# Kernel optimization log

Hardware: AMD Instinct MI355X
Metric: run time of the kernel (lower is better)

Reference implementation:

```python
import jax, jax.numpy as jnp
import numpy as np

N = 50000
R = 8
E = 100000
D_IN = 768
D_H = 256
LN_EPS = 1e-5


def _layer_norm(h, g, b):
    mu = jnp.mean(h, axis=-1, keepdims=True)
    var = jnp.mean((h - mu) ** 2, axis=-1, keepdims=True)
    return (h - mu) * jax.lax.rsqrt(var + LN_EPS) * g + b


def _rgcn_layer(x, node_w, edge_src, edge_tgt, W_rel, W_self_w, W_self_b, ln_g, ln_b):
    # x: [N, d_in]; edge_src/edge_tgt: [R, E]; W_rel: [R, d_in, d_out]
    n = x.shape[0]
    out = x @ W_self_w + W_self_b  # self loop
    for r in range(W_rel.shape[0]):  # fixed, small relation count
        src = edge_src[r]
        tgt = edge_tgt[r]
        feats = x[src] * node_w[src][:, None]          # gather + nuclearity scale, [E, d_in]
        msg = feats @ W_rel[r]                          # per-relation linear, [E, d_out]
        agg = jax.ops.segment_sum(msg, tgt, num_segments=n)                 # scatter_add
        cnt = jax.ops.segment_sum(jnp.ones(src.shape[0], x.dtype), tgt, num_segments=n)
        out = out + agg / jnp.clip(cnt, 1.0)[:, None]  # mean over relation neighbors
    return _layer_norm(jax.nn.relu(out), ln_g, ln_b)   # dropout = identity (eval)


def setup_inputs() -> dict:
    key = jax.random.key(0)
    ks = jax.random.split(key, 10)
    x = jax.random.normal(ks[0], (N, D_IN), dtype=jnp.float32)
    node_weights = jax.random.uniform(ks[1], (N,), dtype=jnp.float32)
    edge_src = jax.random.randint(ks[2], (R, E), 0, N, dtype=jnp.int32)
    edge_tgt = jax.random.randint(ks[3], (R, E), 0, N, dtype=jnp.int32)
    W_rel0 = jax.random.normal(ks[4], (R, D_IN, D_H), dtype=jnp.float32) / np.sqrt(D_IN)
    W_self0_w = jax.random.normal(ks[5], (D_IN, D_H), dtype=jnp.float32) / np.sqrt(D_IN)
    W_self0_b = jnp.zeros((D_H,), jnp.float32)
    W_rel1 = jax.random.normal(ks[6], (R, D_H, D_H), dtype=jnp.float32) / np.sqrt(D_H)
    W_self1_w = jax.random.normal(ks[7], (D_H, D_H), dtype=jnp.float32) / np.sqrt(D_H)
    W_self1_b = jnp.zeros((D_H,), jnp.float32)
    ones = jnp.ones((D_H,), jnp.float32)
    zeros = jnp.zeros((D_H,), jnp.float32)
    return {
        "x": x, "node_weights": node_weights,
        "edge_src": edge_src, "edge_tgt": edge_tgt,
        "W_rel0": W_rel0, "W_self0_w": W_self0_w, "W_self0_b": W_self0_b,
        "ln0_g": ones, "ln0_b": zeros,
        "W_rel1": W_rel1, "W_self1_w": W_self1_w, "W_self1_b": W_self1_b,
        "ln1_g": ones, "ln1_b": zeros,
    }


def reference(x, node_weights, edge_src, edge_tgt,
              W_rel0, W_self0_w, W_self0_b, ln0_g, ln0_b,
              W_rel1, W_self1_w, W_self1_b, ln1_g, ln1_b):
    h = _rgcn_layer(x, node_weights, edge_src, edge_tgt,
                    W_rel0, W_self0_w, W_self0_b, ln0_g, ln0_b)
    h = _rgcn_layer(h, node_weights, edge_src, edge_tgt,
                    W_rel1, W_self1_w, W_self1_b, ln1_g, ln1_b)
    return h  # [N, 256]
```

## Files before the change

### kernel.cpp

```cpp
#include <hip/hip_runtime.h>
#include <stdint.h>

#define N_NODES 50000
#define M_PAD   50048
#define R_REL   8
#define E_EDGES 100000
#define D_IN    768
#define D_H     256
#define N_CAT   2304
#define LN_EPS  1e-5f

#define TILES_N 18
#define TILES_M 391
#define T_TOT   (TILES_N * TILES_M)
#define T_PER_XCD ((T_TOT + 7) / 8)
#define NCHUNK  49
#define EP_STRIDE 68
#define E_PAD_MAX 960000

typedef __attribute__((ext_vector_type(8))) __bf16        bf16x8;
typedef __attribute__((ext_vector_type(4))) float         f32x4;
typedef __attribute__((ext_vector_type(8))) unsigned short u16x8;
typedef __attribute__((ext_vector_type(4))) unsigned short u16x4;
typedef __attribute__((ext_vector_type(4))) int            i32x4;

__device__ __forceinline__ float bf2f(unsigned short u) {
  union { float f; uint32_t i; } c; c.i = ((uint32_t)u) << 16; return c.f;
}
__device__ __forceinline__ unsigned short f2bf(float f) {
  uint32_t x = __float_as_uint(f);
  uint32_t r = (x + 0x7fffu + ((x >> 16) & 1u)) >> 16;
  return (unsigned short)r;
}

__device__ __forceinline__ void gload_lds16(const void* g, uint32_t lds_off) {
  __builtin_amdgcn_global_load_lds(
      (const __attribute__((address_space(1))) void*)(uintptr_t)g,
      (__attribute__((address_space(3))) void*)(uintptr_t)lds_off, 16, 0, 0);
}

__global__ void k_deg(const int* __restrict__ tgt, int* __restrict__ deg) {
  int e = blockIdx.x * 256 + threadIdx.x;
  if (e >= R_REL * E_EDGES) return;
  int r = e / E_EDGES;
  atomicAdd(&deg[r * N_NODES + tgt[e]], 1);
}

__global__ void k_ndeg(const int* __restrict__ deg, int* __restrict__ pdeg) {
  int t = blockIdx.x * 256 + threadIdx.x;
  if (t >= N_NODES) return;
  int s = 0;
#pragma unroll
  for (int r = 0; r < R_REL; ++r) s += deg[r * N_NODES + t];
  pdeg[t] = (s + 3) & ~3;
}

__global__ __launch_bounds__(256)
void k_scan1(const int* __restrict__ deg, int* __restrict__ rowptr,
             int* __restrict__ bsum) {
  __shared__ int wtot[4];
  const int chunk = blockIdx.x, tid = threadIdx.x;
  const int wave = tid >> 6, lane = tid & 63;
  const int i0 = chunk * 1024 + tid * 4;
  int v0 = 0, v1 = 0, v2 = 0, v3 = 0;
  const int* d = deg;
  if (chunk != NCHUNK - 1) {
    i32x4 v = *(const i32x4*)(d + i0);
    v0 = v[0]; v1 = v[1]; v2 = v[2]; v3 = v[3];
  } else {
    if (i0 + 0 < N_NODES) v0 = d[i0 + 0];
    if (i0 + 1 < N_NODES) v1 = d[i0 + 1];
    if (i0 + 2 < N_NODES) v2 = d[i0 + 2];
    if (i0 + 3 < N_NODES) v3 = d[i0 + 3];
  }
  const int tsum = v0 + v1 + v2 + v3;
  int inc = tsum;
#pragma unroll
  for (int off = 1; off < 64; off <<= 1) {
    int t = __shfl_up(inc, off, 64);
    if (lane >= off) inc += t;
  }
  if (lane == 63) wtot[wave] = inc;
  __syncthreads();
  int woff = 0;
#pragma unroll
  for (int w = 0; w < 4; ++w) woff += (w < wave) ? wtot[w] : 0;
  int excl = woff + inc - tsum;
  int* rp = rowptr;
  if (i0 + 0 < N_NODES) rp[i0 + 0] = excl;
  if (i0 + 1 < N_NODES) rp[i0 + 1] = excl + v0;
  if (i0 + 2 < N_NODES) rp[i0 + 2] = excl + v0 + v1;
  if (i0 + 3 < N_NODES) rp[i0 + 3] = excl + v0 + v1 + v2;
  if (tid == 0) bsum[chunk] = wtot[0] + wtot[1] + wtot[2] + wtot[3];
}

__global__ __launch_bounds__(64)
void k_scan2(const int* __restrict__ bsum, int* __restrict__ chunkoff,
             int* __restrict__ rowptr) {
  const int lane = threadIdx.x & 63;
  int v = (lane < NCHUNK) ? bsum[lane] : 0;
  int inc = v;
#pragma unroll
  for (int off = 1; off < 64; off <<= 1) {
    int t = __shfl_up(inc, off, 64);
    if (lane >= off) inc += t;
  }
  if (lane < NCHUNK) chunkoff[lane] = inc - v;
  if (lane == NCHUNK - 1) rowptr[N_NODES] = inc;
}

__global__ __launch_bounds__(256)
void k_scan3(const int* __restrict__ chunkoff, int* __restrict__ rowptr) {
  const int chunk = blockIdx.x;
  if (chunk == 0) return;
  const int off = chunkoff[chunk];
  const int i0 = chunk * 1024 + threadIdx.x * 4;
#pragma unroll
  for (int j = 0; j < 4; ++j)
    if (i0 + j < N_NODES) rowptr[i0 + j] += off;
}

__global__ void k_prep(const int* __restrict__ nodeptr, int2* __restrict__ scN) {
  int t = blockIdx.x * 256 + threadIdx.x;
  if (t >= N_NODES) return;
  scN[t] = make_int2(nodeptr[t], nodeptr[t + 1] - nodeptr[t]);
}

__global__ void k_fill(const int* __restrict__ src, const int* __restrict__ tgt,
                       const float* __restrict__ nw, const int* __restrict__ nodeptr,
                       const int* __restrict__ deg, int* __restrict__ cursor,
                       int2* __restrict__ e2) {
  int e = blockIdx.x * 256 + threadIdx.x;
  if (e >= R_REL * E_EDGES) return;
  int r = e / E_EDGES;
  int t = tgt[e], s = src[e];
  int pos = atomicAdd(&cursor[t], 1);
  int slot = nodeptr[t] + pos;
  float w = nw[s] / (float)deg[r * N_NODES + t];
  e2[slot] = make_int2(s | (r << 16), __float_as_int(w));
}

__global__ void k_cvt_x(const float* __restrict__ x, unsigned short* __restrict__ xb) {
  const size_t i = ((size_t)blockIdx.x * 256 + threadIdx.x) * 4;
  if (i >= (size_t)N_NODES * D_IN) return;
  const f32x4 v = *(const f32x4*)(x + i);
  u16x4 o = { f2bf(v[0]), f2bf(v[1]), f2bf(v[2]), f2bf(v[3]) };
  *(u16x4*)(xb + i) = o;
}

__global__ void k_cvt_w(const float* __restrict__ Ws, const float* __restrict__ Wr,
                        unsigned short* __restrict__ Wt, int K) {
  int idx = blockIdx.x * 256 + threadIdx.x;
  if (idx >= N_CAT * K) return;
  int n = idx / K, k = idx - n * K;
  float v = (n < 256) ? Ws[k * 256 + n]
                      : Wr[(size_t)((n - 256) >> 8) * K * 256 + k * 256 + (n & 255)];
  Wt[idx] = f2bf(v);
}

__global__ __launch_bounds__(256, 2)
void k_gemm(const unsigned short* __restrict__ A, const unsigned short* __restrict__ Bt,
            unsigned short* __restrict__ C, int K) {
  const int tile = (blockIdx.x & 7) * T_PER_XCD + (blockIdx.x >> 3);
  if (tile >= T_TOT) return;
  const int tileM = (tile / TILES_N) * 128;
  const int tileN = (tile % TILES_N) * 128;

  __shared__ __align__(16) char smem[34816];
  const int tid  = threadIdx.x;
  const int wave = tid >> 6, lane = tid & 63;
  const int wm = (wave >> 1) * 64, wn = (wave & 1) * 64;

  f32x4 acc[4][4] = {};

  const int rl = lane >> 3, sl8 = lane & 7;
  const int cch = sl8 ^ rl;
  const int srow = wave * 8 + rl;
  const unsigned short* gA = A  + (size_t)(tileM + srow) * K + cch * 8;
  const unsigned short* gB = Bt + (size_t)(tileN + srow) * K + cch * 8;
  const uint32_t ldsA = (uint32_t)(uintptr_t)smem;
  const uint32_t ldsB = ldsA + 16384;
  const uint32_t lA0 = ldsA + (wave * 8) * 128;
  const uint32_t lB0 = ldsB + (wave * 8) * 128;

  const char* pAb = smem         + (wm + (lane & 15)) * 128;
  const char* pBb = smem + 16384 + (wn + (lane & 15)) * 128;
  const int fph = lane >> 4, x7 = lane & 7;

  const int nk = K >> 6;
  for (int kt = 0; kt < nk; ++kt) {
    const size_t koff = (size_t)kt * 64;
    __syncthreads();
#pragma unroll
    for (int j = 0; j < 4; ++j) {
      gload_lds16(gA + (size_t)j * 32 * K + koff, lA0 + j * 4096);
      gload_lds16(gB + (size_t)j * 32 * K + koff, lB0 + j * 4096);
    }
    __syncthreads();
#pragma unroll
    for (int kk = 0; kk < 2; ++kk) {
      const int sA = ((kk * 4 + fph) ^ x7) * 16;
      bf16x8 af[4], bfr[4];
#pragma unroll
      for (int i = 0; i < 4; ++i) af[i]  = *(const bf16x8*)(pAb + i * 2048 + sA);
#pragma unroll
      for (int j = 0; j < 4; ++j) bfr[j] = *(const bf16x8*)(pBb + j * 2048 + sA);
#pragma unroll
      for (int i = 0; i < 4; ++i)
#pragma unroll
        for (int j = 0; j < 4; ++j)
          acc[i][j] = __builtin_amdgcn_mfma_f32_16x16x32_bf16(af[i], bfr[j], acc[i][j], 0, 0, 0);
    }
  }

  __syncthreads();
  unsigned short* st = (unsigned short*)smem + wave * (64 * EP_STRIDE);
  const int rq = (lane >> 4) * 4, cq = lane & 15;
#pragma unroll
  for (int i = 0; i < 4; ++i)
#pragma unroll
    for (int j = 0; j < 4; ++j)
#pragma unroll
      for (int p = 0; p < 4; ++p)
        st[(i * 16 + rq + p) * EP_STRIDE + j * 16 + cq] = f2bf(acc[i][j][p]);
#pragma unroll
  for (int pass = 0; pass < 8; ++pass) {
    const int row = pass * 8 + (lane >> 3);
    const unsigned short* rp_ = st + row * EP_STRIDE + (lane & 7) * 8;
    u16x4 lo = *(const u16x4*)(rp_);
    u16x4 hi = *(const u16x4*)(rp_ + 4);
    u16x8 v = { lo[0], lo[1], lo[2], lo[3], hi[0], hi[1], hi[2], hi[3] };
    size_t off = (size_t)(tileM + wm + row) * N_CAT + tileN + wn + (lane & 7) * 8;
    *(u16x8*)(C + off) = v;
  }
}

template <int FINAL>
__global__ __launch_bounds__(256)
void k_gather_ln(const unsigned short* __restrict__ Y, const int2* __restrict__ scN,
                 const int2* __restrict__ e2, const float* __restrict__ bias,
                 const float* __restrict__ g, const float* __restrict__ bln,
                 void* __restrict__ out) {
  const int wave = threadIdx.x >> 6, lane = threadIdx.x & 63;
  const int t = blockIdx.x * 4 + wave;
  if (t >= N_NODES) return;
  const int c0 = lane * 4;

  float a0, a1, a2, a3;
  {
    u16x4 sv = *(const u16x4*)(Y + (size_t)t * N_CAT + c0);
    f32x4 bb = *(const f32x4*)(bias + c0);
    a0 = bf2f(sv[0]) + bb[0];
    a1 = bf2f(sv[1]) + bb[1];
    a2 = bf2f(sv[2]) + bb[2];
    a3 = bf2f(sv[3]) + bb[3];
  }

  const int2 s = scN[t];
  const int2* ep = e2 + s.x;
  for (int idx = 0; idx < s.y; idx += 4) {
    const int2 p0 = ep[idx + 0];
    const int2 p1 = ep[idx + 1];
    const int2 p2 = ep[idx + 2];
    const int2 p3 = ep[idx + 3];
    const unsigned short* y0 = Y + (size_t)(p0.x & 0xFFFF) * N_CAT + (((p0.x >> 16) + 1) << 8) + c0;
    const unsigned short* y1 = Y + (size_t)(p1.x & 0xFFFF) * N_CAT + (((p1.x >> 16) + 1) << 8) + c0;
    const unsigned short* y2 = Y + (size_t)(p2.x & 0xFFFF) * N_CAT + (((p2.x >> 16) + 1) << 8) + c0;
    const unsigned short* y3 = Y + (size_t)(p3.x & 0xFFFF) * N_CAT + (((p3.x >> 16) + 1) << 8) + c0;
    u16x4 v0 = *(const u16x4*)y0;
    u16x4 v1 = *(const u16x4*)y1;
    u16x4 v2 = *(const u16x4*)y2;
    u16x4 v3 = *(const u16x4*)y3;
    const float w0 = __int_as_float(p0.y), w1 = __int_as_float(p1.y);
    const float w2 = __int_as_float(p2.y), w3 = __int_as_float(p3.y);
    a0 += w0 * bf2f(v0[0]) + w1 * bf2f(v1[0]) + w2 * bf2f(v2[0]) + w3 * bf2f(v3[0]);
    a1 += w0 * bf2f(v0[1]) + w1 * bf2f(v1[1]) + w2 * bf2f(v2[1]) + w3 * bf2f(v3[1]);
    a2 += w0 * bf2f(v0[2]) + w1 * bf2f(v1[2]) + w2 * bf2f(v2[2]) + w3 * bf2f(v3[2]);
    a3 += w0 * bf2f(v0[3]) + w1 * bf2f(v1[3]) + w2 * bf2f(v2[3]) + w3 * bf2f(v3[3]);
  }

  a0 = fmaxf(a0, 0.f); a1 = fmaxf(a1, 0.f); a2 = fmaxf(a2, 0.f); a3 = fmaxf(a3, 0.f);

  float s1 = (a0 + a1) + (a2 + a3);
#pragma unroll
  for (int off = 32; off > 0; off >>= 1) s1 += __shfl_xor(s1, off, 64);
  const float mu = s1 * (1.f / 256.f);
  const float d0 = a0 - mu, d1 = a1 - mu, d2 = a2 - mu, d3 = a3 - mu;
  float s2 = (d0 * d0 + d1 * d1) + (d2 * d2 + d3 * d3);
#pragma unroll
  for (int off = 32; off > 0; off >>= 1) s2 += __shfl_xor(s2, off, 64);
  const float rs = rsqrtf(s2 * (1.f / 256.f) + LN_EPS);

  f32x4 gg = *(const f32x4*)(g + c0);
  f32x4 ll = *(const f32x4*)(bln + c0);
  const float o0 = d0 * rs * gg[0] + ll[0];
  const float o1 = d1 * rs * gg[1] + ll[1];
  const float o2 = d2 * rs * gg[2] + ll[2];
  const float o3 = d3 * rs * gg[3] + ll[3];
  if (FINAL) {
    f32x4 o = { o0, o1, o2, o3 };
    *(f32x4*)((float*)out + (size_t)t * 256 + c0) = o;
  } else {
    u16x4 o = { f2bf(o0), f2bf(o1), f2bf(o2), f2bf(o3) };
    *(u16x4*)((unsigned short*)out + (size_t)t * 256 + c0) = o;
  }
}

extern "C" void kernel_launch(void* const* d_in, const int* in_sizes, int n_in,
                              void* d_out, int out_size, void* d_ws, size_t ws_size,
                              hipStream_t stream) {
  (void)in_sizes; (void)n_in; (void)out_size; (void)ws_size;
  const float* x   = (const float*)d_in[0];
  const float* nw  = (const float*)d_in[1];
  const int*   esrc = (const int*)d_in[2];
  const int*   etgt = (const int*)d_in[3];
  const float* Wr0 = (const float*)d_in[4];
  const float* Ws0 = (const float*)d_in[5];
  const float* Wb0 = (const float*)d_in[6];
  const float* g0  = (const float*)d_in[7];
  const float* b0  = (const float*)d_in[8];
  const float* Wr1 = (const float*)d_in[9];
  const float* Ws1 = (const float*)d_in[10];
  const float* Wb1 = (const float*)d_in[11];
  const float* g1  = (const float*)d_in[12];
  const float* b1  = (const float*)d_in[13];

  char* p = (char*)d_ws;
  auto carve = [&](size_t bytes) {
    char* q = p;
    p += (bytes + 511) & ~(size_t)511;
    return q;
  };
  unsigned short* Y   = (unsigned short*)carve((size_t)M_PAD * N_CAT * 2);
  unsigned short* xb  = (unsigned short*)carve((size_t)M_PAD * D_IN * 2);
  unsigned short* h   = (unsigned short*)carve((size_t)M_PAD * D_H * 2);
  unsigned short* Wt0 = (unsigned short*)carve((size_t)N_CAT * D_IN * 2);
  unsigned short* Wt1 = (unsigned short*)carve((size_t)N_CAT * D_H * 2);
  int*   deg     = (int*)carve((size_t)R_REL * N_NODES * 4);
  int*   pdeg    = (int*)carve((size_t)N_NODES * 4);
  int*   cursor  = (int*)carve((size_t)N_NODES * 4);
  int*   nodeptr = (int*)carve((size_t)(N_NODES + 1) * 4);
  int*   bsum    = (int*)carve((size_t)NCHUNK * 4);
  int*   chunkoff= (int*)carve((size_t)NCHUNK * 4);
  int2*  e2      = (int2*)carve((size_t)E_PAD_MAX * 8);
  int2*  scN     = (int2*)carve((size_t)N_NODES * 8);

  hipMemsetAsync(deg, 0, (size_t)R_REL * N_NODES * 4, stream);
  hipMemsetAsync(cursor, 0, (size_t)N_NODES * 4, stream);
  hipMemsetAsync(e2, 0, (size_t)E_PAD_MAX * 8, stream);
  k_deg<<<(R_REL * E_EDGES + 255) / 256, 256, 0, stream>>>(etgt, deg);
  k_ndeg<<<(N_NODES + 255) / 256, 256, 0, stream>>>(deg, pdeg);
  k_scan1<<<NCHUNK, 256, 0, stream>>>(pdeg, nodeptr, bsum);
  k_scan2<<<1, 64, 0, stream>>>(bsum, chunkoff, nodeptr);
  k_scan3<<<NCHUNK, 256, 0, stream>>>(chunkoff, nodeptr);
  k_prep<<<(N_NODES + 255) / 256, 256, 0, stream>>>(nodeptr, scN);
  k_fill<<<(R_REL * E_EDGES + 255) / 256, 256, 0, stream>>>(esrc, etgt, nw, nodeptr,
                                                            deg, cursor, e2);
  k_cvt_x<<<(N_NODES * D_IN / 4 + 255) / 256, 256, 0, stream>>>(x, xb);
  k_cvt_w<<<(N_CAT * D_IN + 255) / 256, 256, 0, stream>>>(Ws0, Wr0, Wt0, D_IN);
  k_cvt_w<<<(N_CAT * D_H + 255) / 256, 256, 0, stream>>>(Ws1, Wr1, Wt1, D_H);

  const int nblk = 8 * T_PER_XCD;
  k_gemm<<<nblk, 256, 0, stream>>>(xb, Wt0, Y, D_IN);
  k_gather_ln<0><<<N_NODES / 4, 256, 0, stream>>>(Y, scN, e2, Wb0, g0, b0, h);
  k_gemm<<<nblk, 256, 0, stream>>>(h, Wt1, Y, D_H);
  k_gather_ln<1><<<N_NODES / 4, 256, 0, stream>>>(Y, scN, e2, Wb1, g1, b1, d_out);
}
```

Baseline: 792.7 us.

## Rewrite GEMM as 256x256 double-buffered tile with staged prefetch

```diff
diff --git a/kernel.cpp b/kernel.cpp
--- a/kernel.cpp
+++ b/kernel.cpp
@@ -2,7 +2,7 @@
 #include <stdint.h>
 
 #define N_NODES 50000
-#define M_PAD   50048
+#define M_PAD   50176
 #define R_REL   8
 #define E_EDGES 100000
 #define D_IN    768
@@ -10,10 +10,9 @@
 #define N_CAT   2304
 #define LN_EPS  1e-5f
 
-#define TILES_N 18
-#define TILES_M 391
-#define T_TOT   (TILES_N * TILES_M)
-#define T_PER_XCD ((T_TOT + 7) / 8)
+#define TILES_M256 196
+#define TILES_N256 9
+#define T_TOT256   1764
 #define NCHUNK  49
 #define EP_STRIDE 68
 #define E_PAD_MAX 960000
@@ -158,80 +157,117 @@
   Wt[idx] = f2bf(v);
 }
 
-__global__ __launch_bounds__(256, 2)
+__global__ __launch_bounds__(512, 2)
 void k_gemm(const unsigned short* __restrict__ A, const unsigned short* __restrict__ Bt,
             unsigned short* __restrict__ C, int K) {
-  const int tile = (blockIdx.x & 7) * T_PER_XCD + (blockIdx.x >> 3);
-  if (tile >= T_TOT) return;
-  const int tileM = (tile / TILES_N) * 128;
-  const int tileN = (tile % TILES_N) * 128;
-
-  __shared__ __align__(16) char smem[34816];
+  __shared__ __align__(16) char smem[131072];
+
+  const int bid = blockIdx.x;
+  const int xcd = bid & 7, idx = bid >> 3;
+  const int q9 = T_TOT256 >> 3, rr = T_TOT256 & 7;
+  const int wg = (xcd < rr ? xcd * (q9 + 1)
+                           : rr * (q9 + 1) + (xcd - rr) * q9) + idx;
+  const int tm9 = wg / 9;
+  const int tileM = tm9 * 256;
+  const int tileN = (wg - tm9 * 9) * 256;
+
   const int tid  = threadIdx.x;
   const int wave = tid >> 6, lane = tid & 63;
-  const int wm = (wave >> 1) * 64, wn = (wave & 1) * 64;
-
-  f32x4 acc[4][4] = {};
-
-  const int rl = lane >> 3, sl8 = lane & 7;
-  const int cch = sl8 ^ rl;
-  const int srow = wave * 8 + rl;
-  const unsigned short* gA = A  + (size_t)(tileM + srow) * K + cch * 8;
-  const unsigned short* gB = Bt + (size_t)(tileN + srow) * K + cch * 8;
+  const int wmRow = (wave >> 2) * 128;
+  const int wnRow = (wave & 3) * 64;
+  const int c16 = lane & 15, fph = lane >> 4, x7 = lane & 7;
+
+  const int srow = tid >> 3, sl8 = tid & 7;
+  const int cch = sl8 ^ (srow & 7);
+  const unsigned short* gA0 = A  + (size_t)(tileM + srow) * K + cch * 8;
+  const unsigned short* gB0 = Bt + (size_t)(tileN + srow) * K + cch * 8;
   const uint32_t ldsA = (uint32_t)(uintptr_t)smem;
-  const uint32_t ldsB = ldsA + 16384;
-  const uint32_t lA0 = ldsA + (wave * 8) * 128;
-  const uint32_t lB0 = ldsB + (wave * 8) * 128;
-
-  const char* pAb = smem         + (wm + (lane & 15)) * 128;
-  const char* pBb = smem + 16384 + (wn + (lane & 15)) * 128;
-  const int fph = lane >> 4, x7 = lane & 7;
+  const uint32_t ldsB = ldsA + 65536u;
+  const uint32_t linA = (uint32_t)(srow * 128 + sl8 * 16);
+
+#define STA(R0, tt) gload_lds16(gA0 + (size_t)(R0) * K + (size_t)(tt) * 64, \
+                                ldsA + (uint32_t)(((tt) & 1) * 32768) + (uint32_t)((R0) * 128) + linA)
+#define STB(R0, tt) gload_lds16(gB0 + (size_t)(R0) * K + (size_t)(tt) * 64, \
+                                ldsB + (uint32_t)(((tt) & 1) * 32768) + (uint32_t)((R0) * 128) + linA)
+
+  f32x4 acc[8][4] = {};
+
+  const char* pA = smem          + (wmRow + c16) * 128;
+  const char* pB = smem + 65536  + (wnRow + c16) * 128;
 
   const int nk = K >> 6;
-  for (int kt = 0; kt < nk; ++kt) {
-    const size_t koff = (size_t)kt * 64;
-    __syncthreads();
-#pragma unroll
-    for (int j = 0; j < 4; ++j) {
-      gload_lds16(gA + (size_t)j * 32 * K + koff, lA0 + j * 4096);
-      gload_lds16(gB + (size_t)j * 32 * K + koff, lB0 + j * 4096);
+
+  STA(0, 0); STA(128, 0); STA(64, 0); STA(192, 0);
+  STB(0, 0); STB(64, 0);  STB(128, 0); STB(192, 0);
+  STA(0, 1); STA(128, 1);
+  asm volatile("s_waitcnt vmcnt(2)" ::: "memory");
+  asm volatile("s_barrier" ::: "memory");
+
+  for (int t = 0; t < nk; ++t) {
+    const uint32_t bA = (uint32_t)(t & 1) * 32768u;
+#pragma unroll
+    for (int q = 0; q < 4; ++q) {
+      bf16x8 af[2][2], bfr[2][4];
+#pragma unroll
+      for (int kk = 0; kk < 2; ++kk) {
+        const int sA = ((kk * 4 + fph) ^ x7) * 16;
+#pragma unroll
+        for (int i2 = 0; i2 < 2; ++i2)
+          af[i2][kk] = *(const bf16x8*)(pA + bA + (q * 2 + i2) * 2048 + sA);
+#pragma unroll
+        for (int nj = 0; nj < 4; ++nj)
+          bfr[kk][nj] = *(const bf16x8*)(pB + bA + nj * 2048 + sA);
+      }
+      if (q == 0 && t + 1 < nk) { STA(64, t + 1); STA(192, t + 1); STB(0, t + 1); STB(64, t + 1); }
+      if (q == 1 && t + 1 < nk) { STB(128, t + 1); STB(192, t + 1); }
+      if (q == 2 && t + 2 < nk) { STA(0, t + 2); STA(128, t + 2); }
+      asm volatile("s_barrier" ::: "memory");
+      asm volatile("s_waitcnt lgkmcnt(0)" ::: "memory");
+      __builtin_amdgcn_s_setprio(1);
+#pragma unroll
+      for (int i2 = 0; i2 < 2; ++i2)
+#pragma unroll
+        for (int nj = 0; nj < 4; ++nj)
+#pragma unroll
+          for (int kk = 0; kk < 2; ++kk)
+            acc[q * 2 + i2][nj] = __builtin_amdgcn_mfma_f32_16x16x32_bf16(
+                af[i2][kk], bfr[kk][nj], acc[q * 2 + i2][nj], 0, 0, 0);
+      __builtin_amdgcn_s_setprio(0);
+      if (q < 3) asm volatile("s_barrier" ::: "memory");
     }
-    __syncthreads();
-#pragma unroll
-    for (int kk = 0; kk < 2; ++kk) {
-      const int sA = ((kk * 4 + fph) ^ x7) * 16;
-      bf16x8 af[4], bfr[4];
-#pragma unroll
-      for (int i = 0; i < 4; ++i) af[i]  = *(const bf16x8*)(pAb + i * 2048 + sA);
-#pragma unroll
-      for (int j = 0; j < 4; ++j) bfr[j] = *(const bf16x8*)(pBb + j * 2048 + sA);
-#pragma unroll
-      for (int i = 0; i < 4; ++i)
-#pragma unroll
-        for (int j = 0; j < 4; ++j)
-          acc[i][j] = __builtin_amdgcn_mfma_f32_16x16x32_bf16(af[i], bfr[j], acc[i][j], 0, 0, 0);
+    if (t + 1 < nk) {
+      if (t + 2 < nk) asm volatile("s_waitcnt vmcnt(2)" ::: "memory");
+      else            asm volatile("s_waitcnt vmcnt(0)" ::: "memory");
+      asm volatile("s_barrier" ::: "memory");
     }
   }
-
-  __syncthreads();
+  asm volatile("s_waitcnt vmcnt(0)" ::: "memory");
+  asm volatile("s_barrier" ::: "memory");
+
+#undef STA
+#undef STB
+
   unsigned short* st = (unsigned short*)smem + wave * (64 * EP_STRIDE);
-  const int rq = (lane >> 4) * 4, cq = lane & 15;
-#pragma unroll
-  for (int i = 0; i < 4; ++i)
-#pragma unroll
-    for (int j = 0; j < 4; ++j)
-#pragma unroll
-      for (int p = 0; p < 4; ++p)
-        st[(i * 16 + rq + p) * EP_STRIDE + j * 16 + cq] = f2bf(acc[i][j][p]);
-#pragma unroll
-  for (int pass = 0; pass < 8; ++pass) {
-    const int row = pass * 8 + (lane >> 3);
-    const unsigned short* rp_ = st + row * EP_STRIDE + (lane & 7) * 8;
-    u16x4 lo = *(const u16x4*)(rp_);
-    u16x4 hi = *(const u16x4*)(rp_ + 4);
-    u16x8 v = { lo[0], lo[1], lo[2], lo[3], hi[0], hi[1], hi[2], hi[3] };
-    size_t off = (size_t)(tileM + wm + row) * N_CAT + tileN + wn + (lane & 7) * 8;
-    *(u16x8*)(C + off) = v;
+  const int rq4 = (lane >> 4) * 4, cq = lane & 15;
+#pragma unroll
+  for (int half = 0; half < 2; ++half) {
+#pragma unroll
+    for (int i = 0; i < 4; ++i)
+#pragma unroll
+      for (int j = 0; j < 4; ++j)
+#pragma unroll
+        for (int p = 0; p < 4; ++p)
+          st[(i * 16 + rq4 + p) * EP_STRIDE + j * 16 + cq] = f2bf(acc[half * 4 + i][j][p]);
+#pragma unroll
+    for (int pass = 0; pass < 8; ++pass) {
+      const int row = pass * 8 + (lane >> 3);
+      const unsigned short* rp_ = st + row * EP_STRIDE + (lane & 7) * 8;
+      u16x4 lo = *(const u16x4*)(rp_);
+      u16x4 hi = *(const u16x4*)(rp_ + 4);
+      u16x8 v = { lo[0], lo[1], lo[2], lo[3], hi[0], hi[1], hi[2], hi[3] };
+      size_t off = (size_t)(tileM + wmRow + half * 64 + row) * N_CAT + tileN + wnRow + (lane & 7) * 8;
+      *(u16x8*)(C + off) = v;
+    }
   }
 }
 
@@ -360,9 +396,8 @@
   k_cvt_w<<<(N_CAT * D_IN + 255) / 256, 256, 0, stream>>>(Ws0, Wr0, Wt0, D_IN);
   k_cvt_w<<<(N_CAT * D_H + 255) / 256, 256, 0, stream>>>(Ws1, Wr1, Wt1, D_H);
 
-  const int nblk = 8 * T_PER_XCD;
-  k_gemm<<<nblk, 256, 0, stream>>>(xb, Wt0, Y, D_IN);
+  k_gemm<<<T_TOT256, 512, 0, stream>>>(xb, Wt0, Y, D_IN);
   k_gather_ln<0><<<N_NODES / 4, 256, 0, stream>>>(Y, scN, e2, Wb0, g0, b0, h);
-  k_gemm<<<nblk, 256, 0, stream>>>(h, Wt1, Y, D_H);
+  k_gemm<<<T_TOT256, 512, 0, stream>>>(h, Wt1, Y, D_H);
   k_gather_ln<1><<<N_NODES / 4, 256, 0, stream>>>(Y, scN, e2, Wb1, g1, b1, d_out);
 }
```

Result: slower. 827.8 us (+4.4%).

## Double-buffer GEMM K-loop with K=32 stages and raise occupancy

Applied to the files above, without the earlier changes.

```diff
diff --git a/kernel.cpp b/kernel.cpp
--- a/kernel.cpp
+++ b/kernel.cpp
@@ -2,7 +2,7 @@
 #include <stdint.h>
 
 #define N_NODES 50000
-#define M_PAD   50048
+#define M_PAD   50176
 #define R_REL   8
 #define E_EDGES 100000
 #define D_IN    768
@@ -10,10 +10,10 @@
 #define N_CAT   2304
 #define LN_EPS  1e-5f
 
-#define TILES_N 18
-#define TILES_M 391
-#define T_TOT   (TILES_N * TILES_M)
-#define T_PER_XCD ((T_TOT + 7) / 8)
+#define TILES_M128 392
+#define TILES_N128 18
+#define T_TOT128   7056
+#define CPX128     882
 #define NCHUNK  49
 #define EP_STRIDE 68
 #define E_PAD_MAX 960000
@@ -158,71 +158,87 @@
   Wt[idx] = f2bf(v);
 }
 
-__global__ __launch_bounds__(256, 2)
+__global__ __launch_bounds__(256, 4)
 void k_gemm(const unsigned short* __restrict__ A, const unsigned short* __restrict__ Bt,
             unsigned short* __restrict__ C, int K) {
-  const int tile = (blockIdx.x & 7) * T_PER_XCD + (blockIdx.x >> 3);
-  if (tile >= T_TOT) return;
-  const int tileM = (tile / TILES_N) * 128;
-  const int tileN = (tile % TILES_N) * 128;
-
   __shared__ __align__(16) char smem[34816];
-  const int tid  = threadIdx.x;
-  const int wave = tid >> 6, lane = tid & 63;
+
+  const int bid = blockIdx.x;
+  const int wg = (bid & 7) * CPX128 + (bid >> 3);
+  const int tileM = (wg / TILES_N128) * 128;
+  const int tileN = (wg % TILES_N128) * 128;
+
+  const int tid = threadIdx.x, wave = tid >> 6, lane = tid & 63;
   const int wm = (wave >> 1) * 64, wn = (wave & 1) * 64;
+  const int c16 = lane & 15, fph = lane >> 4;
+
+  const int srow = tid >> 2;
+  const int cch = (tid & 3) ^ ((srow >> 1) & 3);
+  const unsigned short* gAr0 = A  + (size_t)(tileM + srow) * K + cch * 8;
+  const unsigned short* gAr1 = gAr0 + (size_t)64 * K;
+  const unsigned short* gBr0 = Bt + (size_t)(tileN + srow) * K + cch * 8;
+  const unsigned short* gBr1 = gBr0 + (size_t)64 * K;
+  const uint32_t ldsA = (uint32_t)(uintptr_t)smem;
+  const uint32_t ldsB = ldsA + 16384u;
+  const uint32_t lin = (uint32_t)(tid * 16);
 
   f32x4 acc[4][4] = {};
 
-  const int rl = lane >> 3, sl8 = lane & 7;
-  const int cch = sl8 ^ rl;
-  const int srow = wave * 8 + rl;
-  const unsigned short* gA = A  + (size_t)(tileM + srow) * K + cch * 8;
-  const unsigned short* gB = Bt + (size_t)(tileN + srow) * K + cch * 8;
-  const uint32_t ldsA = (uint32_t)(uintptr_t)smem;
-  const uint32_t ldsB = ldsA + 16384;
-  const uint32_t lA0 = ldsA + (wave * 8) * 128;
-  const uint32_t lB0 = ldsB + (wave * 8) * 128;
-
-  const char* pAb = smem         + (wm + (lane & 15)) * 128;
-  const char* pBb = smem + 16384 + (wn + (lane & 15)) * 128;
-  const int fph = lane >> 4, x7 = lane & 7;
-
-  const int nk = K >> 6;
-  for (int kt = 0; kt < nk; ++kt) {
-    const size_t koff = (size_t)kt * 64;
-    __syncthreads();
-#pragma unroll
-    for (int j = 0; j < 4; ++j) {
-      gload_lds16(gA + (size_t)j * 32 * K + koff, lA0 + j * 4096);
-      gload_lds16(gB + (size_t)j * 32 * K + koff, lB0 + j * 4096);
+  const int slot = (fph ^ ((c16 >> 1) & 3)) * 16;
+  const char* pA = smem         + (wm + c16) * 64 + slot;
+  const char* pB = smem + 16384 + (wn + c16) * 64 + slot;
+
+  const int nk = K >> 5;
+
+  gload_lds16(gAr0, ldsA + lin);
+  gload_lds16(gAr1, ldsA + 4096u + lin);
+  gload_lds16(gBr0, ldsB + lin);
+  gload_lds16(gBr1, ldsB + 4096u + lin);
+  asm volatile("s_waitcnt vmcnt(0)" ::: "memory");
+  asm volatile("s_barrier" ::: "memory");
+
+  for (int tp = 0; tp < nk; tp += 2) {
+#pragma unroll
+    for (int u = 0; u < 2; ++u) {
+      const uint32_t par  = u ? 8192u : 0u;
+      const uint32_t parN = u ? 0u : 8192u;
+      const int t = tp + u;
+      if (t + 1 < nk) {
+        const int soff = (u + 1) * 32;
+        gload_lds16(gAr0 + soff, ldsA + parN + lin);
+        gload_lds16(gAr1 + soff, ldsA + parN + 4096u + lin);
+        gload_lds16(gBr0 + soff, ldsB + parN + lin);
+        gload_lds16(gBr1 + soff, ldsB + parN + 4096u + lin);
+      }
+      bf16x8 bfr[4], af[4];
+#pragma unroll
+      for (int nj = 0; nj < 4; ++nj) bfr[nj] = *(const bf16x8*)(pB + par + nj * 1024);
+#pragma unroll
+      for (int mi = 0; mi < 4; ++mi) af[mi]  = *(const bf16x8*)(pA + par + mi * 1024);
+#pragma unroll
+      for (int mi = 0; mi < 4; ++mi)
+#pragma unroll
+        for (int nj = 0; nj < 4; ++nj)
+          acc[mi][nj] = __builtin_amdgcn_mfma_f32_16x16x32_bf16(af[mi], bfr[nj],
+                                                                acc[mi][nj], 0, 0, 0);
+      if (t + 1 < nk) {
+        asm volatile("s_waitcnt vmcnt(0)" ::: "memory");
+        asm volatile("s_barrier" ::: "memory");
+      }
     }
-    __syncthreads();
-#pragma unroll
-    for (int kk = 0; kk < 2; ++kk) {
-      const int sA = ((kk * 4 + fph) ^ x7) * 16;
-      bf16x8 af[4], bfr[4];
-#pragma unroll
-      for (int i = 0; i < 4; ++i) af[i]  = *(const bf16x8*)(pAb + i * 2048 + sA);
-#pragma unroll
-      for (int j = 0; j < 4; ++j) bfr[j] = *(const bf16x8*)(pBb + j * 2048 + sA);
-#pragma unroll
-      for (int i = 0; i < 4; ++i)
-#pragma unroll
-        for (int j = 0; j < 4; ++j)
-          acc[i][j] = __builtin_amdgcn_mfma_f32_16x16x32_bf16(af[i], bfr[j], acc[i][j], 0, 0, 0);
-    }
-  }
-
-  __syncthreads();
+    gAr0 += 64; gAr1 += 64; gBr0 += 64; gBr1 += 64;
+  }
+  asm volatile("s_barrier" ::: "memory");
+
   unsigned short* st = (unsigned short*)smem + wave * (64 * EP_STRIDE);
-  const int rq = (lane >> 4) * 4, cq = lane & 15;
+  const int rq4 = (lane >> 4) * 4, cq = lane & 15;
 #pragma unroll
   for (int i = 0; i < 4; ++i)
 #pragma unroll
     for (int j = 0; j < 4; ++j)
 #pragma unroll
       for (int p = 0; p < 4; ++p)
-        st[(i * 16 + rq + p) * EP_STRIDE + j * 16 + cq] = f2bf(acc[i][j][p]);
+        st[(i * 16 + rq4 + p) * EP_STRIDE + j * 16 + cq] = f2bf(acc[i][j][p]);
 #pragma unroll
   for (int pass = 0; pass < 8; ++pass) {
     const int row = pass * 8 + (lane >> 3);
@@ -360,9 +376,8 @@
   k_cvt_w<<<(N_CAT * D_IN + 255) / 256, 256, 0, stream>>>(Ws0, Wr0, Wt0, D_IN);
   k_cvt_w<<<(N_CAT * D_H + 255) / 256, 256, 0, stream>>>(Ws1, Wr1, Wt1, D_H);
 
-  const int nblk = 8 * T_PER_XCD;
-  k_gemm<<<nblk, 256, 0, stream>>>(xb, Wt0, Y, D_IN);
+  k_gemm<<<T_TOT128, 256, 0, stream>>>(xb, Wt0, Y, D_IN);
   k_gather_ln<0><<<N_NODES / 4, 256, 0, stream>>>(Y, scN, e2, Wb0, g0, b0, h);
-  k_gemm<<<nblk, 256, 0, stream>>>(h, Wt1, Y, D_H);
+  k_gemm<<<T_TOT128, 256, 0, stream>>>(h, Wt1, Y, D_H);
   k_gather_ln<1><<<N_NODES / 4, 256, 0, stream>>>(Y, scN, e2, Wb1, g1, b1, d_out);
 }
```

Result: slower. 815.4 us (+2.9%).
